# Optimization experiments

Measured on AMD Instinct MI355X. Metric: run time of the kernel, lower is better.

## Reference

```python
import jax, jax.numpy as jnp
import numpy as np

NUM_HEADS = 12
WIN = 7  # window_size[0] == window_size[1]


def setup_inputs() -> dict:
    key = jax.random.key(0)
    ks = jax.random.split(key, 8)
    B_, N, C = 2048, WIN * WIN, 384
    nW = 64
    return {
        "x": jax.random.normal(ks[0], (B_, N, C), dtype=jnp.float32),
        "mask": jax.random.normal(ks[1], (nW, N, N), dtype=jnp.float32),
        "qkv_w": jax.random.normal(ks[2], (3 * C, C), dtype=jnp.float32) * 0.02,
        "qkv_b": jax.random.normal(ks[3], (3 * C,), dtype=jnp.float32) * 0.02,
        "proj_w": jax.random.normal(ks[4], (C, C), dtype=jnp.float32) * 0.02,
        "proj_b": jax.random.normal(ks[5], (C,), dtype=jnp.float32) * 0.02,
        "rpb_table": jax.random.normal(ks[6], ((2 * WIN - 1) ** 2, NUM_HEADS), dtype=jnp.float32) * 0.02,
        "rel_index": jax.random.randint(ks[7], (N * N,), 0, (2 * WIN - 1) ** 2, dtype=jnp.int32),
    }


def reference(x, mask, qkv_w, qkv_b, proj_w, proj_b, rpb_table, rel_index):
    B_, N, C = x.shape
    H = NUM_HEADS
    d = C // H
    scale = d ** -0.5

    # QKV projection (quant wrappers act as identity in non-quant state)
    qkv = x @ qkv_w.T + qkv_b                      # [B_, N, 3C]
    qkv = qkv.reshape(B_, N, 3, H, d).transpose(2, 0, 3, 1, 4)  # [3, B_, H, N, d]
    q, k, v = qkv[0], qkv[1], qkv[2]

    attn = jnp.einsum("bhnd,bhmd->bhnm", q * scale, k)  # [B_, H, N, N]

    # relative position bias gather: [N*N] -> [N, N, H] -> [H, N, N]
    bias = rpb_table[rel_index].reshape(N, N, H).transpose(2, 0, 1)
    attn = attn + bias[None]

    # shifted-window mask add
    nW = mask.shape[0]
    attn = attn.reshape(B_ // nW, nW, H, N, N) + mask[None, :, None]
    attn = attn.reshape(B_, H, N, N)

    attn = jax.nn.softmax(attn, axis=-1)

    out = jnp.einsum("bhnm,bhmd->bhnd", attn, v)   # [B_, H, N, d]
    out = out.transpose(0, 2, 1, 3).reshape(B_, N, C)
    out = out @ proj_w.T + proj_b
    return out, attn
```

## Files before the change

### kernel.cpp

```cpp
#include <hip/hip_runtime.h>
#include <hip/hip_bf16.h>
#include <stdint.h>

#define H_ 12
#define D_ 32
#define N_ 49
#define C_ 384
#define B_TOT 2048
#define BH 24576
#define M_ROWS 100352
#define SCALE 0.17677669529663689f

typedef float f32x4 __attribute__((ext_vector_type(4)));
typedef __bf16 bf16x8 __attribute__((ext_vector_type(8)));
typedef unsigned short ushortx8 __attribute__((ext_vector_type(8)));

static __device__ __forceinline__ unsigned short f2bf(float f) {
  __bf16 b = (__bf16)f;
  return __builtin_bit_cast(unsigned short, b);
}

__global__ void cast_bf16(const float* __restrict__ in,
                          unsigned short* __restrict__ out, int n8) {
  int i = blockIdx.x * blockDim.x + threadIdx.x;
  const int stride = gridDim.x * blockDim.x;
  for (; i < n8; i += stride) {
    float4 a = ((const float4*)in)[2 * i];
    float4 b = ((const float4*)in)[2 * i + 1];
    ushortx8 v;
    v[0] = f2bf(a.x); v[1] = f2bf(a.y); v[2] = f2bf(a.z); v[3] = f2bf(a.w);
    v[4] = f2bf(b.x); v[5] = f2bf(b.y); v[6] = f2bf(b.z); v[7] = f2bf(b.w);
    *(ushortx8*)&out[(size_t)i * 8] = v;
  }
}

__global__ void build_comb(const float* __restrict__ mask,
                           const float* __restrict__ rpb,
                           const int* __restrict__ ridx,
                           float* __restrict__ comb) {
  const int h = blockIdx.x, w = blockIdx.y;
  float* cb = comb + (size_t)(w * H_ + h) * 4096;
  const float* mw = mask + (size_t)w * N_ * N_;
  for (int e = threadIdx.x; e < 4096; e += 256) {
    const int r = e >> 6, c = e & 63;
    float v;
    if (c >= N_) v = -1e30f;
    else if (r >= N_) v = 0.0f;
    else v = mw[r * N_ + c] + rpb[ridx[r * N_ + c] * H_ + h];
    cb[e] = v;
  }
}

__global__ __launch_bounds__(256, 3)
void qkv_gemm(const unsigned short* __restrict__ A,
              const unsigned short* __restrict__ W,
              const float* __restrict__ bias, unsigned short* __restrict__ qkv) {
  __shared__ __align__(16) unsigned short smem[20480];
  unsigned short* lA0 = smem;
  unsigned short* lB0 = smem + 10240;
  const int tid = threadIdx.x;
  const int w = blockIdx.x;
  const int t = (w & 7) * 882 + (w >> 3);
  const int bm = t / 9, bn = t - bm * 9;

  const int lane = tid & 63, wv = tid >> 6;
  const int wm = wv >> 1, wn = wv & 1;
  const int lo = lane & 15, hi = lane >> 4;
  const int r0 = tid >> 2, r1 = r0 + 64;
  const int off = (tid & 3) * 8;

  const unsigned short* Ab = A + (size_t)bm * 128 * 384;
  const unsigned short* Wb = W + (size_t)bn * 128 * 384;

  f32x4 acc[4][4];
#pragma unroll
  for (int i = 0; i < 4; i++)
#pragma unroll
    for (int j = 0; j < 4; j++)
#pragma unroll
      for (int r = 0; r < 4; r++) acc[i][j][r] = 0.0f;

  *(uint4*)&lA0[r0 * 40 + off] = *(const uint4*)(Ab + r0 * 384 + off);
  *(uint4*)&lA0[r1 * 40 + off] = *(const uint4*)(Ab + r1 * 384 + off);
  *(uint4*)&lB0[r0 * 40 + off] = *(const uint4*)(Wb + r0 * 384 + off);
  *(uint4*)&lB0[r1 * 40 + off] = *(const uint4*)(Wb + r1 * 384 + off);
  __syncthreads();

  int buf = 0;
  for (int kt = 0; kt < 12; kt++) {
    uint4 pa0, pa1, pb0, pb1;
    if (kt < 11) {
      const int kc = (kt + 1) * 32 + off;
      pa0 = *(const uint4*)(Ab + r0 * 384 + kc);
      pa1 = *(const uint4*)(Ab + r1 * 384 + kc);
      pb0 = *(const uint4*)(Wb + r0 * 384 + kc);
      pb1 = *(const uint4*)(Wb + r1 * 384 + kc);
    }
    const unsigned short* la = lA0 + buf * 5120;
    const unsigned short* lb = lB0 + buf * 5120;
    bf16x8 af[4], bfm[4];
#pragma unroll
    for (int mt = 0; mt < 4; mt++)
      af[mt] = *(const bf16x8*)&la[(wm * 64 + mt * 16 + lo) * 40 + hi * 8];
#pragma unroll
    for (int nt = 0; nt < 4; nt++)
      bfm[nt] = *(const bf16x8*)&lb[(wn * 64 + nt * 16 + lo) * 40 + hi * 8];
#pragma unroll
    for (int mt = 0; mt < 4; mt++)
#pragma unroll
      for (int nt = 0; nt < 4; nt++)
        acc[mt][nt] = __builtin_amdgcn_mfma_f32_16x16x32_bf16(af[mt], bfm[nt], acc[mt][nt], 0, 0, 0);
    if (kt < 11) {
      unsigned short* wa = lA0 + (buf ^ 1) * 5120;
      unsigned short* wb = lB0 + (buf ^ 1) * 5120;
      *(uint4*)&wa[r0 * 40 + off] = pa0;
      *(uint4*)&wa[r1 * 40 + off] = pa1;
      *(uint4*)&wb[r0 * 40 + off] = pb0;
      *(uint4*)&wb[r1 * 40 + off] = pb1;
    }
    __syncthreads();
    buf ^= 1;
  }

  unsigned short* ep = smem + wv * 5120;
#pragma unroll
  for (int nt = 0; nt < 4; nt++) {
    const int j = bn * 128 + wn * 64 + nt * 16 + lo;
    const float bj = bias[j];
    const float mul = (j < 384) ? SCALE : 1.0f;
    const int ch = nt >> 1;
    const int dd = (nt & 1) * 16 + lo;
#pragma unroll
    for (int mt = 0; mt < 4; mt++) {
#pragma unroll
      for (int r = 0; r < 4; r++) {
        const int row = mt * 16 + hi * 4 + r;
        ep[(row * 2 + ch) * 40 + dd] = f2bf((acc[mt][nt][r] + bj) * mul);
      }
    }
  }
#pragma unroll
  for (int cc = 0; cc < 2; cc++) {
    const int cidx = cc * 64 + lane;
    const int lr = cidx >> 1, lch = cidx & 1;
    const int i = bm * 128 + wm * 64 + lr;
    const int b = i / 49, sq = i - b * 49;
    const int j0 = bn * 128 + wn * 64 + lch * 32;
    const int which = j0 / 384;
    const int rem = j0 - which * 384;
    const int h = rem >> 5;
    unsigned short* dst = qkv + ((size_t)which * BH + (size_t)b * H_ + h) * (N_ * D_) + sq * D_;
    const unsigned short* src = ep + cidx * 40;
#pragma unroll
    for (int q = 0; q < 4; q++)
      *(uint4*)(dst + q * 8) = *(const uint4*)(src + q * 8);
  }
}

__global__ __launch_bounds__(64, 2)
void attn_kernel(const unsigned short* __restrict__ qkv,
                 const float* __restrict__ comb,
                 float* __restrict__ probs,
                 unsigned short* __restrict__ av) {
  __shared__ __align__(16) unsigned short P[64 * 72];
  __shared__ __align__(16) unsigned short VT[32 * 72];
  const int lane = threadIdx.x;
  const int lo = lane & 15, hi = lane >> 4;
  const int h = blockIdx.x, b = blockIdx.y;

  const unsigned short* qp = qkv + (size_t)(b * H_ + h) * (N_ * D_);
  const unsigned short* kp = qp + (size_t)BH * (N_ * D_);
  const unsigned short* vp = kp + (size_t)BH * (N_ * D_);

  {
    unsigned int* vz = (unsigned int*)VT;
#pragma unroll
    for (int i = 0; i < 18; i++) vz[lane + 64 * i] = 0u;
  }
  __syncthreads();

  bf16x8 aq[4], bk[4];
#pragma unroll
  for (int t = 0; t < 4; t++) {
    aq[t] = *(const bf16x8*)(qp + (t * 16 + lo) * D_ + hi * 8);
    bk[t] = *(const bf16x8*)(kp + (t * 16 + lo) * D_ + hi * 8);
  }
  f32x4 s[4][4];
#pragma unroll
  for (int mt = 0; mt < 4; mt++)
#pragma unroll
    for (int nt = 0; nt < 4; nt++) {
#pragma unroll
      for (int r = 0; r < 4; r++) s[mt][nt][r] = 0.0f;
      s[mt][nt] = __builtin_amdgcn_mfma_f32_16x16x32_bf16(aq[mt], bk[nt], s[mt][nt], 0, 0, 0);
    }

#pragma unroll
  for (int it = 0; it < 4; it++) {
    const int idx = it * 64 + lane;
    if (idx < 196) {
      const int sq = idx >> 2, ch = idx & 3;
      ushortx8 vv = *(const ushortx8*)(vp + sq * D_ + ch * 8);
#pragma unroll
      for (int jj = 0; jj < 8; jj++) VT[(ch * 8 + jj) * 72 + sq] = vv[jj];
    }
  }

  const float* cb = comb + (size_t)((b & 63) * H_ + h) * 4096;
#pragma unroll
  for (int mt = 0; mt < 4; mt++) {
#pragma unroll
    for (int r = 0; r < 4; r++) {
      const int row = mt * 16 + hi * 4 + r;
      const float* crow = cb + row * 64 + lo;
      float v0 = s[mt][0][r] + crow[0];
      float v1 = s[mt][1][r] + crow[16];
      float v2 = s[mt][2][r] + crow[32];
      float v3 = s[mt][3][r] + crow[48];
      float m = fmaxf(fmaxf(v0, v1), fmaxf(v2, v3));
      m = fmaxf(m, __shfl_xor(m, 1));
      m = fmaxf(m, __shfl_xor(m, 2));
      m = fmaxf(m, __shfl_xor(m, 4));
      m = fmaxf(m, __shfl_xor(m, 8));
      v0 = __expf(v0 - m); v1 = __expf(v1 - m);
      v2 = __expf(v2 - m); v3 = __expf(v3 - m);
      float sum = v0 + v1 + v2 + v3;
      sum += __shfl_xor(sum, 1);
      sum += __shfl_xor(sum, 2);
      sum += __shfl_xor(sum, 4);
      sum += __shfl_xor(sum, 8);
      const float rinv = 1.0f / sum;
      s[mt][0][r] = v0 * rinv; s[mt][1][r] = v1 * rinv;
      s[mt][2][r] = v2 * rinv; s[mt][3][r] = v3 * rinv;
    }
  }

  const size_t pbase = (size_t)(b * H_ + h) * N_ * N_;
#pragma unroll
  for (int mt = 0; mt < 4; mt++) {
#pragma unroll
    for (int r = 0; r < 4; r++) {
      const int row = mt * 16 + hi * 4 + r;
      if (row < N_) {
#pragma unroll
        for (int nt = 0; nt < 4; nt++) {
          const int c = nt * 16 + lo;
          if (c < N_) probs[pbase + row * N_ + c] = s[mt][nt][r];
        }
      }
#pragma unroll
      for (int nt = 0; nt < 4; nt++)
        P[row * 72 + nt * 16 + lo] = f2bf(s[mt][nt][r]);
    }
  }
  __syncthreads();

  f32x4 o[4][2];
#pragma unroll
  for (int mt = 0; mt < 4; mt++)
#pragma unroll
    for (int n2 = 0; n2 < 2; n2++)
#pragma unroll
      for (int r = 0; r < 4; r++) o[mt][n2][r] = 0.0f;
#pragma unroll
  for (int ks = 0; ks < 2; ks++) {
    bf16x8 pa[4], vb[2];
#pragma unroll
    for (int mt = 0; mt < 4; mt++)
      pa[mt] = *(const bf16x8*)&P[(mt * 16 + lo) * 72 + ks * 32 + hi * 8];
#pragma unroll
    for (int n2 = 0; n2 < 2; n2++)
      vb[n2] = *(const bf16x8*)&VT[(n2 * 16 + lo) * 72 + ks * 32 + hi * 8];
#pragma unroll
    for (int mt = 0; mt < 4; mt++)
#pragma unroll
      for (int n2 = 0; n2 < 2; n2++)
        o[mt][n2] = __builtin_amdgcn_mfma_f32_16x16x32_bf16(pa[mt], vb[n2], o[mt][n2], 0, 0, 0);
  }

  __syncthreads();
#pragma unroll
  for (int mt = 0; mt < 4; mt++) {
#pragma unroll
    for (int r = 0; r < 4; r++) {
      const int row = mt * 16 + hi * 4 + r;
      if (row < N_) {
#pragma unroll
        for (int n2 = 0; n2 < 2; n2++)
          P[row * 40 + n2 * 16 + lo] = f2bf(o[mt][n2][r]);
      }
    }
  }
  if (lane < N_) {
    unsigned short* dst = av + ((size_t)b * N_ + lane) * C_ + h * D_;
    const unsigned short* src = P + lane * 40;
#pragma unroll
    for (int q = 0; q < 4; q++)
      *(uint4*)(dst + q * 8) = *(const uint4*)(src + q * 8);
  }
}

__global__ __launch_bounds__(256, 3)
void proj_gemm(const unsigned short* __restrict__ A,
               const unsigned short* __restrict__ W,
               const float* __restrict__ bias, float* __restrict__ out) {
  __shared__ unsigned short lA[2][128 * 40];
  __shared__ unsigned short lB[2][128 * 40];
  const int tid = threadIdx.x;
  const int w = blockIdx.x;
  const int t = (w & 7) * 294 + (w >> 3);
  const int bm = t / 3, bn = t - bm * 3;
  const int lane = tid & 63, wv = tid >> 6;
  const int wm = wv >> 1, wn = wv & 1;
  const int lo = lane & 15, hi = lane >> 4;
  const int r0 = tid >> 2, r1 = r0 + 64;
  const int off = (tid & 3) * 8;

  const unsigned short* Ab = A + (size_t)bm * 128 * 384;
  const unsigned short* Wb = W + (size_t)bn * 128 * 384;

  f32x4 acc[4][4];
#pragma unroll
  for (int i = 0; i < 4; i++)
#pragma unroll
    for (int j = 0; j < 4; j++)
#pragma unroll
      for (int r = 0; r < 4; r++) acc[i][j][r] = 0.0f;

  *(uint4*)&lA[0][r0 * 40 + off] = *(const uint4*)(Ab + r0 * 384 + off);
  *(uint4*)&lA[0][r1 * 40 + off] = *(const uint4*)(Ab + r1 * 384 + off);
  *(uint4*)&lB[0][r0 * 40 + off] = *(const uint4*)(Wb + r0 * 384 + off);
  *(uint4*)&lB[0][r1 * 40 + off] = *(const uint4*)(Wb + r1 * 384 + off);
  __syncthreads();

  int buf = 0;
  for (int kt = 0; kt < 12; kt++) {
    uint4 pa0, pa1, pb0, pb1;
    if (kt < 11) {
      const int kc = (kt + 1) * 32 + off;
      pa0 = *(const uint4*)(Ab + r0 * 384 + kc);
      pa1 = *(const uint4*)(Ab + r1 * 384 + kc);
      pb0 = *(const uint4*)(Wb + r0 * 384 + kc);
      pb1 = *(const uint4*)(Wb + r1 * 384 + kc);
    }
    bf16x8 af[4], bfm[4];
#pragma unroll
    for (int mt = 0; mt < 4; mt++)
      af[mt] = *(const bf16x8*)&lA[buf][(wm * 64 + mt * 16 + lo) * 40 + hi * 8];
#pragma unroll
    for (int nt = 0; nt < 4; nt++)
      bfm[nt] = *(const bf16x8*)&lB[buf][(wn * 64 + nt * 16 + lo) * 40 + hi * 8];
#pragma unroll
    for (int mt = 0; mt < 4; mt++)
#pragma unroll
      for (int nt = 0; nt < 4; nt++)
        acc[mt][nt] = __builtin_amdgcn_mfma_f32_16x16x32_bf16(af[mt], bfm[nt], acc[mt][nt], 0, 0, 0);
    if (kt < 11) {
      *(uint4*)&lA[buf ^ 1][r0 * 40 + off] = pa0;
      *(uint4*)&lA[buf ^ 1][r1 * 40 + off] = pa1;
      *(uint4*)&lB[buf ^ 1][r0 * 40 + off] = pb0;
      *(uint4*)&lB[buf ^ 1][r1 * 40 + off] = pb1;
    }
    __syncthreads();
    buf ^= 1;
  }

#pragma unroll
  for (int nt = 0; nt < 4; nt++) {
    const int j = bn * 128 + wn * 64 + nt * 16 + lo;
    const float bj = bias[j];
#pragma unroll
    for (int mt = 0; mt < 4; mt++) {
#pragma unroll
      for (int r = 0; r < 4; r++) {
        const int i = bm * 128 + wm * 64 + mt * 16 + hi * 4 + r;
        out[(size_t)i * 384 + j] = acc[mt][nt][r] + bj;
      }
    }
  }
}

extern "C" void kernel_launch(void* const* d_in, const int* in_sizes, int n_in,
                              void* d_out, int out_size, void* d_ws, size_t ws_size,
                              hipStream_t stream) {
  const float* x      = (const float*)d_in[0];
  const float* mask   = (const float*)d_in[1];
  const float* qkv_w  = (const float*)d_in[2];
  const float* qkv_b  = (const float*)d_in[3];
  const float* proj_w = (const float*)d_in[4];
  const float* proj_b = (const float*)d_in[5];
  const float* rpb    = (const float*)d_in[6];
  const int*   ridx   = (const int*)d_in[7];

  unsigned short* qkv   = (unsigned short*)d_ws;
  unsigned short* av    = qkv + (size_t)3 * BH * N_ * D_;
  unsigned short* x_bf  = av;
  float* comb           = (float*)(av + (size_t)M_ROWS * C_);
  unsigned short* wq_bf = (unsigned short*)(comb + 768 * 4096);
  unsigned short* wp_bf = wq_bf + 1152 * 384;
  float* out   = (float*)d_out;
  float* probs = out + (size_t)M_ROWS * C_;

  cast_bf16<<<2048, 256, 0, stream>>>(x, x_bf, M_ROWS * C_ / 8);
  cast_bf16<<<216, 256, 0, stream>>>(qkv_w, wq_bf, 1152 * 384 / 8);
  cast_bf16<<<72, 256, 0, stream>>>(proj_w, wp_bf, 384 * 384 / 8);
  build_comb<<<dim3(H_, 64), 256, 0, stream>>>(mask, rpb, ridx, comb);
  qkv_gemm<<<7056, 256, 0, stream>>>(x_bf, wq_bf, qkv_b, qkv);
  attn_kernel<<<dim3(H_, B_TOT), 64, 0, stream>>>(qkv, comb, probs, av);
  proj_gemm<<<2352, 256, 0, stream>>>(av, wp_bf, proj_b, out);
}
```

Baseline: 480.3 us.

## Fuse attention and output projection into one per-window kernel

Replaces the separate attention kernel and projection GEMM with a single kernel that handles one window per block. Six waves each process two heads and write their bf16 attention output into a swizzled LDS tile, then cooperatively run the projection GEMM from LDS, reading weights straight from global memory. This is meant to remove the global write and re-read of the intermediate attention-output tensor and one kernel launch. In exchange it needs about 130KB of LDS per block, which allows roughly one block per CU and so lowers occupancy. The weight matrix is also re-fetched by every block through the cache without LDS staging.

```diff
diff --git a/kernel.cpp b/kernel.cpp
--- a/kernel.cpp
+++ b/kernel.cpp
@@ -157,224 +157,190 @@
   }
 }
 
-__global__ __launch_bounds__(64, 2)
-void attn_kernel(const unsigned short* __restrict__ qkv,
-                 const float* __restrict__ comb,
-                 float* __restrict__ probs,
-                 unsigned short* __restrict__ av) {
-  __shared__ __align__(16) unsigned short P[64 * 72];
-  __shared__ __align__(16) unsigned short VT[32 * 72];
-  const int lane = threadIdx.x;
+__global__ __launch_bounds__(384, 1)
+void attn_proj(const unsigned short* __restrict__ qkv,
+               const float* __restrict__ comb,
+               const unsigned short* __restrict__ wp,
+               const float* __restrict__ pbias,
+               float* __restrict__ probs,
+               float* __restrict__ out) {
+  __shared__ __align__(16) unsigned short avl[64 * 384];
+  __shared__ __align__(16) unsigned short Pw[6][64 * 72];
+  __shared__ __align__(16) unsigned short VTw[6][32 * 72];
+  const int tid = threadIdx.x;
+  const int wv = tid / 64, lane = tid & 63;
   const int lo = lane & 15, hi = lane >> 4;
-  const int h = blockIdx.x, b = blockIdx.y;
-
-  const unsigned short* qp = qkv + (size_t)(b * H_ + h) * (N_ * D_);
-  const unsigned short* kp = qp + (size_t)BH * (N_ * D_);
-  const unsigned short* vp = kp + (size_t)BH * (N_ * D_);
+  const int b = blockIdx.x;
+
+  unsigned short* P = Pw[wv];
+  unsigned short* VT = VTw[wv];
 
   {
     unsigned int* vz = (unsigned int*)VT;
 #pragma unroll
     for (int i = 0; i < 18; i++) vz[lane + 64 * i] = 0u;
   }
+
+#pragma unroll
+  for (int hh = 0; hh < 2; hh++) {
+    const int h = wv * 2 + hh;
+    const unsigned short* qp = qkv + (size_t)(b * H_ + h) * (N_ * D_);
+    const unsigned short* kp = qp + (size_t)BH * (N_ * D_);
+    const unsigned short* vp = kp + (size_t)BH * (N_ * D_);
+
+    bf16x8 aq[4], bk[4];
+#pragma unroll
+    for (int t = 0; t < 4; t++) {
+      aq[t] = *(const bf16x8*)(qp + (t * 16 + lo) * D_ + hi * 8);
+      bk[t] = *(const bf16x8*)(kp + (t * 16 + lo) * D_ + hi * 8);
+    }
+    f32x4 s[4][4];
+#pragma unroll
+    for (int mt = 0; mt < 4; mt++)
+#pragma unroll
+      for (int nt = 0; nt < 4; nt++) {
+#pragma unroll
+        for (int r = 0; r < 4; r++) s[mt][nt][r] = 0.0f;
+        s[mt][nt] = __builtin_amdgcn_mfma_f32_16x16x32_bf16(aq[mt], bk[nt], s[mt][nt], 0, 0, 0);
+      }
+
+#pragma unroll
+    for (int it = 0; it < 4; it++) {
+      const int idx = it * 64 + lane;
+      if (idx < 196) {
+        const int sq = idx >> 2, ch = idx & 3;
+        ushortx8 vv = *(const ushortx8*)(vp + sq * D_ + ch * 8);
+#pragma unroll
+        for (int jj = 0; jj < 8; jj++) VT[(ch * 8 + jj) * 72 + sq] = vv[jj];
+      }
+    }
+
+    const float* cb = comb + (size_t)((b & 63) * H_ + h) * 4096;
+#pragma unroll
+    for (int mt = 0; mt < 4; mt++) {
+#pragma unroll
+      for (int r = 0; r < 4; r++) {
+        const int row = mt * 16 + hi * 4 + r;
+        const float* crow = cb + row * 64 + lo;
+        float v0 = s[mt][0][r] + crow[0];
+        float v1 = s[mt][1][r] + crow[16];
+        float v2 = s[mt][2][r] + crow[32];
+        float v3 = s[mt][3][r] + crow[48];
+        float m = fmaxf(fmaxf(v0, v1), fmaxf(v2, v3));
+        m = fmaxf(m, __shfl_xor(m, 1));
+        m = fmaxf(m, __shfl_xor(m, 2));
+        m = fmaxf(m, __shfl_xor(m, 4));
+        m = fmaxf(m, __shfl_xor(m, 8));
+        v0 = __expf(v0 - m); v1 = __expf(v1 - m);
+        v2 = __expf(v2 - m); v3 = __expf(v3 - m);
+        float sum = v0 + v1 + v2 + v3;
+        sum += __shfl_xor(sum, 1);
+        sum += __shfl_xor(sum, 2);
+        sum += __shfl_xor(sum, 4);
+        sum += __shfl_xor(sum, 8);
+        const float rinv = 1.0f / sum;
+        s[mt][0][r] = v0 * rinv; s[mt][1][r] = v1 * rinv;
+        s[mt][2][r] = v2 * rinv; s[mt][3][r] = v3 * rinv;
+      }
+    }
+
+    const size_t pbase = (size_t)(b * H_ + h) * N_ * N_;
+#pragma unroll
+    for (int mt = 0; mt < 4; mt++) {
+#pragma unroll
+      for (int r = 0; r < 4; r++) {
+        const int row = mt * 16 + hi * 4 + r;
+        if (row < N_) {
+#pragma unroll
+          for (int nt = 0; nt < 4; nt++) {
+            const int c = nt * 16 + lo;
+            if (c < N_) probs[pbase + row * N_ + c] = s[mt][nt][r];
+          }
+        }
+#pragma unroll
+        for (int nt = 0; nt < 4; nt++)
+          P[row * 72 + nt * 16 + lo] = f2bf(s[mt][nt][r]);
+      }
+    }
+
+    f32x4 o[4][2];
+#pragma unroll
+    for (int mt = 0; mt < 4; mt++)
+#pragma unroll
+      for (int n2 = 0; n2 < 2; n2++)
+#pragma unroll
+        for (int r = 0; r < 4; r++) o[mt][n2][r] = 0.0f;
+#pragma unroll
+    for (int ks = 0; ks < 2; ks++) {
+      bf16x8 pa[4], vb[2];
+#pragma unroll
+      for (int mt = 0; mt < 4; mt++)
+        pa[mt] = *(const bf16x8*)&P[(mt * 16 + lo) * 72 + ks * 32 + hi * 8];
+#pragma unroll
+      for (int n2 = 0; n2 < 2; n2++)
+        vb[n2] = *(const bf16x8*)&VT[(n2 * 16 + lo) * 72 + ks * 32 + hi * 8];
+#pragma unroll
+      for (int mt = 0; mt < 4; mt++)
+#pragma unroll
+        for (int n2 = 0; n2 < 2; n2++)
+          o[mt][n2] = __builtin_amdgcn_mfma_f32_16x16x32_bf16(pa[mt], vb[n2], o[mt][n2], 0, 0, 0);
+    }
+
+#pragma unroll
+    for (int mt = 0; mt < 4; mt++) {
+#pragma unroll
+      for (int r = 0; r < 4; r++) {
+        const int row = mt * 16 + hi * 4 + r;
+#pragma unroll
+        for (int n2 = 0; n2 < 2; n2++) {
+          const int col = h * 32 + n2 * 16 + lo;
+          const int chn = ((col >> 3) ^ (row & 7));
+          avl[row * 384 + chn * 8 + (col & 7)] = f2bf(o[mt][n2][r]);
+        }
+      }
+    }
+  }
+
   __syncthreads();
 
-  bf16x8 aq[4], bk[4];
-#pragma unroll
-  for (int t = 0; t < 4; t++) {
-    aq[t] = *(const bf16x8*)(qp + (t * 16 + lo) * D_ + hi * 8);
-    bk[t] = *(const bf16x8*)(kp + (t * 16 + lo) * D_ + hi * 8);
-  }
-  f32x4 s[4][4];
-#pragma unroll
-  for (int mt = 0; mt < 4; mt++)
-#pragma unroll
-    for (int nt = 0; nt < 4; nt++) {
-#pragma unroll
-      for (int r = 0; r < 4; r++) s[mt][nt][r] = 0.0f;
-      s[mt][nt] = __builtin_amdgcn_mfma_f32_16x16x32_bf16(aq[mt], bk[nt], s[mt][nt], 0, 0, 0);
-    }
-
-#pragma unroll
-  for (int it = 0; it < 4; it++) {
-    const int idx = it * 64 + lane;
-    if (idx < 196) {
-      const int sq = idx >> 2, ch = idx & 3;
-      ushortx8 vv = *(const ushortx8*)(vp + sq * D_ + ch * 8);
-#pragma unroll
-      for (int jj = 0; jj < 8; jj++) VT[(ch * 8 + jj) * 72 + sq] = vv[jj];
-    }
-  }
-
-  const float* cb = comb + (size_t)((b & 63) * H_ + h) * 4096;
-#pragma unroll
-  for (int mt = 0; mt < 4; mt++) {
-#pragma unroll
-    for (int r = 0; r < 4; r++) {
-      const int row = mt * 16 + hi * 4 + r;
-      const float* crow = cb + row * 64 + lo;
-      float v0 = s[mt][0][r] + crow[0];
-      float v1 = s[mt][1][r] + crow[16];
-      float v2 = s[mt][2][r] + crow[32];
-      float v3 = s[mt][3][r] + crow[48];
-      float m = fmaxf(fmaxf(v0, v1), fmaxf(v2, v3));
-      m = fmaxf(m, __shfl_xor(m, 1));
-      m = fmaxf(m, __shfl_xor(m, 2));
-      m = fmaxf(m, __shfl_xor(m, 4));
-      m = fmaxf(m, __shfl_xor(m, 8));
-      v0 = __expf(v0 - m); v1 = __expf(v1 - m);
-      v2 = __expf(v2 - m); v3 = __expf(v3 - m);
-      float sum = v0 + v1 + v2 + v3;
-      sum += __shfl_xor(sum, 1);
-      sum += __shfl_xor(sum, 2);
-      sum += __shfl_xor(sum, 4);
-      sum += __shfl_xor(sum, 8);
-      const float rinv = 1.0f / sum;
-      s[mt][0][r] = v0 * rinv; s[mt][1][r] = v1 * rinv;
-      s[mt][2][r] = v2 * rinv; s[mt][3][r] = v3 * rinv;
-    }
-  }
-
-  const size_t pbase = (size_t)(b * H_ + h) * N_ * N_;
-#pragma unroll
-  for (int mt = 0; mt < 4; mt++) {
-#pragma unroll
-    for (int r = 0; r < 4; r++) {
-      const int row = mt * 16 + hi * 4 + r;
-      if (row < N_) {
-#pragma unroll
-        for (int nt = 0; nt < 4; nt++) {
-          const int c = nt * 16 + lo;
-          if (c < N_) probs[pbase + row * N_ + c] = s[mt][nt][r];
-        }
-      }
+  const int jb = wv * 64;
+  f32x4 acc[4][4];
+#pragma unroll
+  for (int i = 0; i < 4; i++)
+#pragma unroll
+    for (int j = 0; j < 4; j++)
+#pragma unroll
+      for (int r = 0; r < 4; r++) acc[i][j][r] = 0.0f;
+
+  for (int kt = 0; kt < 12; kt++) {
+    bf16x8 af[4], bf[4];
+#pragma unroll
+    for (int mt = 0; mt < 4; mt++) {
+      const int row = mt * 16 + lo;
+      const int chn = ((kt * 4 + hi) ^ (row & 7));
+      af[mt] = *(const bf16x8*)&avl[row * 384 + chn * 8];
+    }
+#pragma unroll
+    for (int nt = 0; nt < 4; nt++)
+      bf[nt] = *(const bf16x8*)(wp + (size_t)(jb + nt * 16 + lo) * 384 + kt * 32 + hi * 8);
+#pragma unroll
+    for (int mt = 0; mt < 4; mt++)
 #pragma unroll
       for (int nt = 0; nt < 4; nt++)
-        P[row * 72 + nt * 16 + lo] = f2bf(s[mt][nt][r]);
-    }
-  }
-  __syncthreads();
-
-  f32x4 o[4][2];
-#pragma unroll
-  for (int mt = 0; mt < 4; mt++)
-#pragma unroll
-    for (int n2 = 0; n2 < 2; n2++)
-#pragma unroll
-      for (int r = 0; r < 4; r++) o[mt][n2][r] = 0.0f;
-#pragma unroll
-  for (int ks = 0; ks < 2; ks++) {
-    bf16x8 pa[4], vb[2];
-#pragma unroll
-    for (int mt = 0; mt < 4; mt++)
-      pa[mt] = *(const bf16x8*)&P[(mt * 16 + lo) * 72 + ks * 32 + hi * 8];
-#pragma unroll
-    for (int n2 = 0; n2 < 2; n2++)
-      vb[n2] = *(const bf16x8*)&VT[(n2 * 16 + lo) * 72 + ks * 32 + hi * 8];
-#pragma unroll
-    for (int mt = 0; mt < 4; mt++)
-#pragma unroll
-      for (int n2 = 0; n2 < 2; n2++)
-        o[mt][n2] = __builtin_amdgcn_mfma_f32_16x16x32_bf16(pa[mt], vb[n2], o[mt][n2], 0, 0, 0);
-  }
-
-  __syncthreads();
-#pragma unroll
-  for (int mt = 0; mt < 4; mt++) {
-#pragma unroll
-    for (int r = 0; r < 4; r++) {
-      const int row = mt * 16 + hi * 4 + r;
-      if (row < N_) {
-#pragma unroll
-        for (int n2 = 0; n2 < 2; n2++)
-          P[row * 40 + n2 * 16 + lo] = f2bf(o[mt][n2][r]);
-      }
-    }
-  }
-  if (lane < N_) {
-    unsigned short* dst = av + ((size_t)b * N_ + lane) * C_ + h * D_;
-    const unsigned short* src = P + lane * 40;
-#pragma unroll
-    for (int q = 0; q < 4; q++)
-      *(uint4*)(dst + q * 8) = *(const uint4*)(src + q * 8);
-  }
-}
-
-__global__ __launch_bounds__(256, 3)
-void proj_gemm(const unsigned short* __restrict__ A,
-               const unsigned short* __restrict__ W,
-               const float* __restrict__ bias, float* __restrict__ out) {
-  __shared__ unsigned short lA[2][128 * 40];
-  __shared__ unsigned short lB[2][128 * 40];
-  const int tid = threadIdx.x;
-  const int w = blockIdx.x;
-  const int t = (w & 7) * 294 + (w >> 3);
-  const int bm = t / 3, bn = t - bm * 3;
-  const int lane = tid & 63, wv = tid >> 6;
-  const int wm = wv >> 1, wn = wv & 1;
-  const int lo = lane & 15, hi = lane >> 4;
-  const int r0 = tid >> 2, r1 = r0 + 64;
-  const int off = (tid & 3) * 8;
-
-  const unsigned short* Ab = A + (size_t)bm * 128 * 384;
-  const unsigned short* Wb = W + (size_t)bn * 128 * 384;
-
-  f32x4 acc[4][4];
-#pragma unroll
-  for (int i = 0; i < 4; i++)
-#pragma unroll
-    for (int j = 0; j < 4; j++)
-#pragma unroll
-      for (int r = 0; r < 4; r++) acc[i][j][r] = 0.0f;
-
-  *(uint4*)&lA[0][r0 * 40 + off] = *(const uint4*)(Ab + r0 * 384 + off);
-  *(uint4*)&lA[0][r1 * 40 + off] = *(const uint4*)(Ab + r1 * 384 + off);
-  *(uint4*)&lB[0][r0 * 40 + off] = *(const uint4*)(Wb + r0 * 384 + off);
-  *(uint4*)&lB[0][r1 * 40 + off] = *(const uint4*)(Wb + r1 * 384 + off);
-  __syncthreads();
-
-  int buf = 0;
-  for (int kt = 0; kt < 12; kt++) {
-    uint4 pa0, pa1, pb0, pb1;
-    if (kt < 11) {
-      const int kc = (kt + 1) * 32 + off;
-      pa0 = *(const uint4*)(Ab + r0 * 384 + kc);
-      pa1 = *(const uint4*)(Ab + r1 * 384 + kc);
-      pb0 = *(const uint4*)(Wb + r0 * 384 + kc);
-      pb1 = *(const uint4*)(Wb + r1 * 384 + kc);
-    }
-    bf16x8 af[4], bfm[4];
-#pragma unroll
-    for (int mt = 0; mt < 4; mt++)
-      af[mt] = *(const bf16x8*)&lA[buf][(wm * 64 + mt * 16 + lo) * 40 + hi * 8];
-#pragma unroll
-    for (int nt = 0; nt < 4; nt++)
-      bfm[nt] = *(const bf16x8*)&lB[buf][(wn * 64 + nt * 16 + lo) * 40 + hi * 8];
-#pragma unroll
-    for (int mt = 0; mt < 4; mt++)
-#pragma unroll
-      for (int nt = 0; nt < 4; nt++)
-        acc[mt][nt] = __builtin_amdgcn_mfma_f32_16x16x32_bf16(af[mt], bfm[nt], acc[mt][nt], 0, 0, 0);
-    if (kt < 11) {
-      *(uint4*)&lA[buf ^ 1][r0 * 40 + off] = pa0;
-      *(uint4*)&lA[buf ^ 1][r1 * 40 + off] = pa1;
-      *(uint4*)&lB[buf ^ 1][r0 * 40 + off] = pb0;
-      *(uint4*)&lB[buf ^ 1][r1 * 40 + off] = pb1;
-    }
-    __syncthreads();
-    buf ^= 1;
+        acc[mt][nt] = __builtin_amdgcn_mfma_f32_16x16x32_bf16(af[mt], bf[nt], acc[mt][nt], 0, 0, 0);
   }
 
 #pragma unroll
   for (int nt = 0; nt < 4; nt++) {
-    const int j = bn * 128 + wn * 64 + nt * 16 + lo;
-    const float bj = bias[j];
-#pragma unroll
-    for (int mt = 0; mt < 4; mt++) {
-#pragma unroll
-      for (int r = 0; r < 4; r++) {
-        const int i = bm * 128 + wm * 64 + mt * 16 + hi * 4 + r;
-        out[(size_t)i * 384 + j] = acc[mt][nt][r] + bj;
+    const int j = jb + nt * 16 + lo;
+    const float bj = pbias[j];
+#pragma unroll
+    for (int mt = 0; mt < 4; mt++) {
+#pragma unroll
+      for (int r = 0; r < 4; r++) {
+        const int row = mt * 16 + hi * 4 + r;
+        if (row < N_)
+          out[((size_t)b * N_ + row) * C_ + j] = acc[mt][nt][r] + bj;
       }
     }
   }
@@ -393,9 +359,8 @@
   const int*   ridx   = (const int*)d_in[7];
 
   unsigned short* qkv   = (unsigned short*)d_ws;
-  unsigned short* av    = qkv + (size_t)3 * BH * N_ * D_;
-  unsigned short* x_bf  = av;
-  float* comb           = (float*)(av + (size_t)M_ROWS * C_);
+  unsigned short* x_bf  = qkv + (size_t)3 * BH * N_ * D_;
+  float* comb           = (float*)(x_bf + (size_t)M_ROWS * C_);
   unsigned short* wq_bf = (unsigned short*)(comb + 768 * 4096);
   unsigned short* wp_bf = wq_bf + 1152 * 384;
   float* out   = (float*)d_out;
@@ -406,6 +371,5 @@
   cast_bf16<<<72, 256, 0, stream>>>(proj_w, wp_bf, 384 * 384 / 8);
   build_comb<<<dim3(H_, 64), 256, 0, stream>>>(mask, rpb, ridx, comb);
   qkv_gemm<<<7056, 256, 0, stream>>>(x_bf, wq_bf, qkv_b, qkv);
-  attn_kernel<<<dim3(H_, B_TOT), 64, 0, stream>>>(qkv, comb, probs, av);
-  proj_gemm<<<2352, 256, 0, stream>>>(av, wp_bf, proj_b, out);
-}
+  attn_proj<<<2048, 384, 0, stream>>>(qkv, comb, wp_bf, proj_b, probs, out);
+}
```

Result: no change. 486.8 us (+1.3%).

## Use direct global-to-LDS loads with XOR swizzle in GEMMs and fuse prep kernels

Applied to the files above, without the earlier changes.

Both GEMM kernels now copy tiles straight from global memory into LDS with global_load_lds, which skips the register staging and separate LDS stores. The padded LDS layout is replaced by an XOR-swizzled unpadded layout to avoid bank conflicts, and the smaller LDS footprint lets occupancy rise to 4 blocks per CU. The four preprocessing launches (casts and the combined bias/mask build) are merged into one kernel to cut launch overhead. The trade-off is that correctness depends on the swizzle matching the fragment reads and on the asynchronous LDS writes being visible at each barrier.

```diff
diff --git a/kernel.cpp b/kernel.cpp
--- a/kernel.cpp
+++ b/kernel.cpp
@@ -20,54 +20,76 @@
   return __builtin_bit_cast(unsigned short, b);
 }
 
-__global__ void cast_bf16(const float* __restrict__ in,
-                          unsigned short* __restrict__ out, int n8) {
-  int i = blockIdx.x * blockDim.x + threadIdx.x;
-  const int stride = gridDim.x * blockDim.x;
-  for (; i < n8; i += stride) {
-    float4 a = ((const float4*)in)[2 * i];
-    float4 b = ((const float4*)in)[2 * i + 1];
+#define GL16(gp, lp)                                                        \
+  __builtin_amdgcn_global_load_lds(                                         \
+      (const __attribute__((address_space(1))) unsigned int*)(gp),          \
+      (__attribute__((address_space(3))) unsigned int*)(lp), 16, 0, 0)
+
+__global__ void prep(const float* __restrict__ x, const float* __restrict__ wq,
+                     const float* __restrict__ wpw, const float* __restrict__ mask,
+                     const float* __restrict__ rpb, const int* __restrict__ ridx,
+                     unsigned short* __restrict__ x_bf,
+                     unsigned short* __restrict__ wq_bf,
+                     unsigned short* __restrict__ wp_bf,
+                     float* __restrict__ comb) {
+  const int blk = blockIdx.x, tid = threadIdx.x;
+  if (blk < 2048) {
+    for (int i = blk * 256 + tid; i < 4816896; i += 2048 * 256) {
+      float4 a = ((const float4*)x)[2 * i];
+      float4 b = ((const float4*)x)[2 * i + 1];
+      ushortx8 v;
+      v[0] = f2bf(a.x); v[1] = f2bf(a.y); v[2] = f2bf(a.z); v[3] = f2bf(a.w);
+      v[4] = f2bf(b.x); v[5] = f2bf(b.y); v[6] = f2bf(b.z); v[7] = f2bf(b.w);
+      *(ushortx8*)&x_bf[(size_t)i * 8] = v;
+    }
+  } else if (blk < 2264) {
+    const int i = (blk - 2048) * 256 + tid;
+    float4 a = ((const float4*)wq)[2 * i];
+    float4 b = ((const float4*)wq)[2 * i + 1];
     ushortx8 v;
     v[0] = f2bf(a.x); v[1] = f2bf(a.y); v[2] = f2bf(a.z); v[3] = f2bf(a.w);
     v[4] = f2bf(b.x); v[5] = f2bf(b.y); v[6] = f2bf(b.z); v[7] = f2bf(b.w);
-    *(ushortx8*)&out[(size_t)i * 8] = v;
-  }
-}
-
-__global__ void build_comb(const float* __restrict__ mask,
-                           const float* __restrict__ rpb,
-                           const int* __restrict__ ridx,
-                           float* __restrict__ comb) {
-  const int h = blockIdx.x, w = blockIdx.y;
-  float* cb = comb + (size_t)(w * H_ + h) * 4096;
-  const float* mw = mask + (size_t)w * N_ * N_;
-  for (int e = threadIdx.x; e < 4096; e += 256) {
-    const int r = e >> 6, c = e & 63;
-    float v;
-    if (c >= N_) v = -1e30f;
-    else if (r >= N_) v = 0.0f;
-    else v = mw[r * N_ + c] + rpb[ridx[r * N_ + c] * H_ + h];
-    cb[e] = v;
-  }
-}
-
-__global__ __launch_bounds__(256, 3)
+    *(ushortx8*)&wq_bf[(size_t)i * 8] = v;
+  } else if (blk < 2336) {
+    const int i = (blk - 2264) * 256 + tid;
+    float4 a = ((const float4*)wpw)[2 * i];
+    float4 b = ((const float4*)wpw)[2 * i + 1];
+    ushortx8 v;
+    v[0] = f2bf(a.x); v[1] = f2bf(a.y); v[2] = f2bf(a.z); v[3] = f2bf(a.w);
+    v[4] = f2bf(b.x); v[5] = f2bf(b.y); v[6] = f2bf(b.z); v[7] = f2bf(b.w);
+    *(ushortx8*)&wp_bf[(size_t)i * 8] = v;
+  } else {
+    const int wh = blk - 2336;
+    const int w = wh / 12, h = wh - w * 12;
+    float* cb = comb + (size_t)wh * 4096;
+    const float* mw = mask + (size_t)w * N_ * N_;
+    for (int e = tid; e < 4096; e += 256) {
+      const int r = e >> 6, c = e & 63;
+      float v;
+      if (c >= N_) v = -1e30f;
+      else if (r >= N_) v = 0.0f;
+      else v = mw[r * N_ + c] + rpb[ridx[r * N_ + c] * H_ + h];
+      cb[e] = v;
+    }
+  }
+}
+
+__global__ __launch_bounds__(256, 4)
 void qkv_gemm(const unsigned short* __restrict__ A,
               const unsigned short* __restrict__ W,
               const float* __restrict__ bias, unsigned short* __restrict__ qkv) {
-  __shared__ __align__(16) unsigned short smem[20480];
-  unsigned short* lA0 = smem;
-  unsigned short* lB0 = smem + 10240;
+  __shared__ __align__(16) unsigned short smem[16384];
   const int tid = threadIdx.x;
   const int w = blockIdx.x;
   const int t = (w & 7) * 882 + (w >> 3);
   const int bm = t / 9, bn = t - bm * 9;
-
   const int lane = tid & 63, wv = tid >> 6;
   const int wm = wv >> 1, wn = wv & 1;
   const int lo = lane & 15, hi = lane >> 4;
-  const int r0 = tid >> 2, r1 = r0 + 64;
-  const int off = (tid & 3) * 8;
+
+  const int sr0 = tid >> 2, sq0 = (tid & 3) ^ ((sr0 >> 1) & 3);
+  const int ci1 = tid + 256;
+  const int sr1 = ci1 >> 2, sq1 = (ci1 & 3) ^ ((sr1 >> 1) & 3);
 
   const unsigned short* Ab = A + (size_t)bm * 128 * 384;
   const unsigned short* Wb = W + (size_t)bn * 128 * 384;
@@ -80,62 +102,60 @@
 #pragma unroll
       for (int r = 0; r < 4; r++) acc[i][j][r] = 0.0f;
 
-  *(uint4*)&lA0[r0 * 40 + off] = *(const uint4*)(Ab + r0 * 384 + off);
-  *(uint4*)&lA0[r1 * 40 + off] = *(const uint4*)(Ab + r1 * 384 + off);
-  *(uint4*)&lB0[r0 * 40 + off] = *(const uint4*)(Wb + r0 * 384 + off);
-  *(uint4*)&lB0[r1 * 40 + off] = *(const uint4*)(Wb + r1 * 384 + off);
+  {
+    unsigned short* b0 = smem;
+    GL16(Ab + sr0 * 384 + sq0 * 8, b0 + tid * 8);
+    GL16(Ab + sr1 * 384 + sq1 * 8, b0 + ci1 * 8);
+    GL16(Wb + sr0 * 384 + sq0 * 8, b0 + 4096 + tid * 8);
+    GL16(Wb + sr1 * 384 + sq1 * 8, b0 + 4096 + ci1 * 8);
+  }
   __syncthreads();
 
   int buf = 0;
   for (int kt = 0; kt < 12; kt++) {
-    uint4 pa0, pa1, pb0, pb1;
     if (kt < 11) {
-      const int kc = (kt + 1) * 32 + off;
-      pa0 = *(const uint4*)(Ab + r0 * 384 + kc);
-      pa1 = *(const uint4*)(Ab + r1 * 384 + kc);
-      pb0 = *(const uint4*)(Wb + r0 * 384 + kc);
-      pb1 = *(const uint4*)(Wb + r1 * 384 + kc);
-    }
-    const unsigned short* la = lA0 + buf * 5120;
-    const unsigned short* lb = lB0 + buf * 5120;
+      const int kk = (kt + 1) * 32;
+      unsigned short* nb = smem + (buf ^ 1) * 8192;
+      GL16(Ab + sr0 * 384 + kk + sq0 * 8, nb + tid * 8);
+      GL16(Ab + sr1 * 384 + kk + sq1 * 8, nb + ci1 * 8);
+      GL16(Wb + sr0 * 384 + kk + sq0 * 8, nb + 4096 + tid * 8);
+      GL16(Wb + sr1 * 384 + kk + sq1 * 8, nb + 4096 + ci1 * 8);
+    }
+    const unsigned short* ba = smem + buf * 8192;
     bf16x8 af[4], bfm[4];
 #pragma unroll
-    for (int mt = 0; mt < 4; mt++)
-      af[mt] = *(const bf16x8*)&la[(wm * 64 + mt * 16 + lo) * 40 + hi * 8];
-#pragma unroll
-    for (int nt = 0; nt < 4; nt++)
-      bfm[nt] = *(const bf16x8*)&lb[(wn * 64 + nt * 16 + lo) * 40 + hi * 8];
+    for (int mt = 0; mt < 4; mt++) {
+      const int row = wm * 64 + mt * 16 + lo;
+      af[mt] = *(const bf16x8*)&ba[(row * 4 + (hi ^ ((row >> 1) & 3))) * 8];
+    }
+#pragma unroll
+    for (int nt = 0; nt < 4; nt++) {
+      const int row = wn * 64 + nt * 16 + lo;
+      bfm[nt] = *(const bf16x8*)&ba[4096 + (row * 4 + (hi ^ ((row >> 1) & 3))) * 8];
+    }
 #pragma unroll
     for (int mt = 0; mt < 4; mt++)
 #pragma unroll
       for (int nt = 0; nt < 4; nt++)
         acc[mt][nt] = __builtin_amdgcn_mfma_f32_16x16x32_bf16(af[mt], bfm[nt], acc[mt][nt], 0, 0, 0);
-    if (kt < 11) {
-      unsigned short* wa = lA0 + (buf ^ 1) * 5120;
-      unsigned short* wb = lB0 + (buf ^ 1) * 5120;
-      *(uint4*)&wa[r0 * 40 + off] = pa0;
-      *(uint4*)&wa[r1 * 40 + off] = pa1;
-      *(uint4*)&wb[r0 * 40 + off] = pb0;
-      *(uint4*)&wb[r1 * 40 + off] = pb1;
-    }
     __syncthreads();
     buf ^= 1;
   }
 
-  unsigned short* ep = smem + wv * 5120;
+  unsigned short* ep = smem + wv * 4096;
 #pragma unroll
   for (int nt = 0; nt < 4; nt++) {
     const int j = bn * 128 + wn * 64 + nt * 16 + lo;
     const float bj = bias[j];
     const float mul = (j < 384) ? SCALE : 1.0f;
-    const int ch = nt >> 1;
-    const int dd = (nt & 1) * 16 + lo;
+    const int c16 = nt * 2 + (lo >> 3);
+    const int wi = lo & 7;
 #pragma unroll
     for (int mt = 0; mt < 4; mt++) {
 #pragma unroll
       for (int r = 0; r < 4; r++) {
         const int row = mt * 16 + hi * 4 + r;
-        ep[(row * 2 + ch) * 40 + dd] = f2bf((acc[mt][nt][r] + bj) * mul);
+        ep[row * 64 + ((c16 ^ hi) << 3) + wi] = f2bf((acc[mt][nt][r] + bj) * mul);
       }
     }
   }
@@ -149,11 +169,13 @@
     const int which = j0 / 384;
     const int rem = j0 - which * 384;
     const int h = rem >> 5;
+    const int hlr = (lr >> 2) & 3;
     unsigned short* dst = qkv + ((size_t)which * BH + (size_t)b * H_ + h) * (N_ * D_) + sq * D_;
-    const unsigned short* src = ep + cidx * 40;
-#pragma unroll
-    for (int q = 0; q < 4; q++)
-      *(uint4*)(dst + q * 8) = *(const uint4*)(src + q * 8);
+#pragma unroll
+    for (int q = 0; q < 4; q++) {
+      const int c16r = lch * 4 + q;
+      *(uint4*)(dst + q * 8) = *(const uint4*)&ep[lr * 64 + ((c16r ^ hlr) << 3)];
+    }
   }
 }
 
@@ -300,12 +322,11 @@
   }
 }
 
-__global__ __launch_bounds__(256, 3)
+__global__ __launch_bounds__(256, 4)
 void proj_gemm(const unsigned short* __restrict__ A,
                const unsigned short* __restrict__ W,
                const float* __restrict__ bias, float* __restrict__ out) {
-  __shared__ unsigned short lA[2][128 * 40];
-  __shared__ unsigned short lB[2][128 * 40];
+  __shared__ __align__(16) unsigned short smem[16384];
   const int tid = threadIdx.x;
   const int w = blockIdx.x;
   const int t = (w & 7) * 294 + (w >> 3);
@@ -313,8 +334,10 @@
   const int lane = tid & 63, wv = tid >> 6;
   const int wm = wv >> 1, wn = wv & 1;
   const int lo = lane & 15, hi = lane >> 4;
-  const int r0 = tid >> 2, r1 = r0 + 64;
-  const int off = (tid & 3) * 8;
+
+  const int sr0 = tid >> 2, sq0 = (tid & 3) ^ ((sr0 >> 1) & 3);
+  const int ci1 = tid + 256;
+  const int sr1 = ci1 >> 2, sq1 = (ci1 & 3) ^ ((sr1 >> 1) & 3);
 
   const unsigned short* Ab = A + (size_t)bm * 128 * 384;
   const unsigned short* Wb = W + (size_t)bn * 128 * 384;
@@ -327,40 +350,42 @@
 #pragma unroll
       for (int r = 0; r < 4; r++) acc[i][j][r] = 0.0f;
 
-  *(uint4*)&lA[0][r0 * 40 + off] = *(const uint4*)(Ab + r0 * 384 + off);
-  *(uint4*)&lA[0][r1 * 40 + off] = *(const uint4*)(Ab + r1 * 384 + off);
-  *(uint4*)&lB[0][r0 * 40 + off] = *(const uint4*)(Wb + r0 * 384 + off);
-  *(uint4*)&lB[0][r1 * 40 + off] = *(const uint4*)(Wb + r1 * 384 + off);
+  {
+    unsigned short* b0 = smem;
+    GL16(Ab + sr0 * 384 + sq0 * 8, b0 + tid * 8);
+    GL16(Ab + sr1 * 384 + sq1 * 8, b0 + ci1 * 8);
+    GL16(Wb + sr0 * 384 + sq0 * 8, b0 + 4096 + tid * 8);
+    GL16(Wb + sr1 * 384 + sq1 * 8, b0 + 4096 + ci1 * 8);
+  }
   __syncthreads();
 
   int buf = 0;
   for (int kt = 0; kt < 12; kt++) {
-    uint4 pa0, pa1, pb0, pb1;
     if (kt < 11) {
-      const int kc = (kt + 1) * 32 + off;
-      pa0 = *(const uint4*)(Ab + r0 * 384 + kc);
-      pa1 = *(const uint4*)(Ab + r1 * 384 + kc);
-      pb0 = *(const uint4*)(Wb + r0 * 384 + kc);
-      pb1 = *(const uint4*)(Wb + r1 * 384 + kc);
-    }
+      const int kk = (kt + 1) * 32;
+      unsigned short* nb = smem + (buf ^ 1) * 8192;
+      GL16(Ab + sr0 * 384 + kk + sq0 * 8, nb + tid * 8);
+      GL16(Ab + sr1 * 384 + kk + sq1 * 8, nb + ci1 * 8);
+      GL16(Wb + sr0 * 384 + kk + sq0 * 8, nb + 4096 + tid * 8);
+      GL16(Wb + sr1 * 384 + kk + sq1 * 8, nb + 4096 + ci1 * 8);
+    }
+    const unsigned short* ba = smem + buf * 8192;
     bf16x8 af[4], bfm[4];
 #pragma unroll
-    for (int mt = 0; mt < 4; mt++)
-      af[mt] = *(const bf16x8*)&lA[buf][(wm * 64 + mt * 16 + lo) * 40 + hi * 8];
-#pragma unroll
-    for (int nt = 0; nt < 4; nt++)
-      bfm[nt] = *(const bf16x8*)&lB[buf][(wn * 64 + nt * 16 + lo) * 40 + hi * 8];
+    for (int mt = 0; mt < 4; mt++) {
+      const int row = wm * 64 + mt * 16 + lo;
+      af[mt] = *(const bf16x8*)&ba[(row * 4 + (hi ^ ((row >> 1) & 3))) * 8];
+    }
+#pragma unroll
+    for (int nt = 0; nt < 4; nt++) {
+      const int row = wn * 64 + nt * 16 + lo;
+      bfm[nt] = *(const bf16x8*)&ba[4096 + (row * 4 + (hi ^ ((row >> 1) & 3))) * 8];
+    }
 #pragma unroll
     for (int mt = 0; mt < 4; mt++)
 #pragma unroll
       for (int nt = 0; nt < 4; nt++)
         acc[mt][nt] = __builtin_amdgcn_mfma_f32_16x16x32_bf16(af[mt], bfm[nt], acc[mt][nt], 0, 0, 0);
-    if (kt < 11) {
-      *(uint4*)&lA[buf ^ 1][r0 * 40 + off] = pa0;
-      *(uint4*)&lA[buf ^ 1][r1 * 40 + off] = pa1;
-      *(uint4*)&lB[buf ^ 1][r0 * 40 + off] = pb0;
-      *(uint4*)&lB[buf ^ 1][r1 * 40 + off] = pb1;
-    }
     __syncthreads();
     buf ^= 1;
   }
@@ -393,18 +418,16 @@
   const int*   ridx   = (const int*)d_in[7];
 
   unsigned short* qkv   = (unsigned short*)d_ws;
-  unsigned short* av    = qkv + (size_t)3 * BH * N_ * D_;
-  unsigned short* x_bf  = av;
-  float* comb           = (float*)(av + (size_t)M_ROWS * C_);
+  unsigned short* x_bf  = qkv + (size_t)3 * BH * N_ * D_;
+  unsigned short* av    = x_bf;
+  float* comb           = (float*)(x_bf + (size_t)M_ROWS * C_);
   unsigned short* wq_bf = (unsigned short*)(comb + 768 * 4096);
   unsigned short* wp_bf = wq_bf + 1152 * 384;
   float* out   = (float*)d_out;
   float* probs = out + (size_t)M_ROWS * C_;
 
-  cast_bf16<<<2048, 256, 0, stream>>>(x, x_bf, M_ROWS * C_ / 8);
-  cast_bf16<<<216, 256, 0, stream>>>(qkv_w, wq_bf, 1152 * 384 / 8);
-  cast_bf16<<<72, 256, 0, stream>>>(proj_w, wp_bf, 384 * 384 / 8);
-  build_comb<<<dim3(H_, 64), 256, 0, stream>>>(mask, rpb, ridx, comb);
+  prep<<<3104, 256, 0, stream>>>(x, qkv_w, proj_w, mask, rpb, ridx,
+                                 x_bf, wq_bf, wp_bf, comb);
   qkv_gemm<<<7056, 256, 0, stream>>>(x_bf, wq_bf, qkv_b, qkv);
   attn_kernel<<<dim3(H_, B_TOT), 64, 0, stream>>>(qkv, comb, probs, av);
   proj_gemm<<<2352, 256, 0, stream>>>(av, wp_bf, proj_b, out);
```

New measurement: 459.4 us. -4.4%, faster.
